# Kernel optimization log

Hardware: AMD Instinct MI355X
Metric: run time of the kernel (lower is better)

## Reference

```python
import jax, jax.numpy as jnp
import numpy as np

F = 8        # number of fields
N_SEQ = 2    # first N_SEQ fields are sequence features
B = 4096     # batch
L = 50       # sequence length for sequence fields
V = 100000   # vocab per field
E = 64       # emb_dim


def setup_inputs() -> dict:
    key = jax.random.key(0)
    k1, k2, k3 = jax.random.split(key, 3)
    x_seq = jax.random.randint(k1, (N_SEQ, B, L), 0, V)          # sequence field inputs
    x_cat = jax.random.randint(k2, (F - N_SEQ, B, 1), 0, V)      # categorical field inputs
    # packed pair-wise tables: tables[a, t] is the embedding table for field a
    # when interacting with target field t (diagonal a==t is unused).
    # RandomNormal(stddev=0.01) initializer in the original.
    tables = jax.random.normal(k3, (F, F, V, E), dtype=jnp.float32) * 0.01
    return {"x_seq": x_seq, "x_cat": x_cat, "tables": tables}


def _pooled(tables, x_seq, x_cat):
    # P[a, t] in [B, E]: field a's input embedded with table (a -> t),
    # mean-pooled over the sequence axis (keepdims semantics folded in).
    P = []
    for a in range(F):  # small fixed loop over fields (structurally distinct inputs)
        idx = x_seq[a] if a < N_SEQ else x_cat[a - N_SEQ]   # [B, La]
        emb = jnp.take(tables[a], idx, axis=1)              # [F, B, La, E]
        P.append(emb.mean(axis=2))                          # [F, B, E]
    return jnp.stack(P)                                     # [F(src), F(tgt), B, E]


def reference(x_seq, x_cat, tables):
    P = _pooled(tables, x_seq, x_cat)
    iu, ju = np.triu_indices(F, k=1)  # all unordered field pairs (a < b)
    # sum over pairs of <emb_{a->b}(x_a), emb_{b->a}(x_b)>
    out = jnp.einsum('pbe,pbe->b', P[iu, ju], P[ju, iu])     # [B]
    return out[:, None, None]                                # [B, 1, 1], matching tf.matmul output
```

## Files before the change

### kernel.cpp

```cpp
#include <hip/hip_runtime.h>

#define FQ 8
#define NSEQ 2
#define BQ 4096
#define LQ 50
#define VQ 100000
#define EQ 64
#define NPAIR 28
#define CQ 4
#define CHUNKS (BQ / CQ)

__device__ const int PA[NPAIR] = {0,0,0,0,0,0,0, 1,1,1,1,1,1, 2,2,2,2,2, 3,3,3,3, 4,4,4, 5,5, 6};
__device__ const int PB[NPAIR] = {1,2,3,4,5,6,7, 2,3,4,5,6,7, 3,4,5,6,7, 4,5,6,7, 5,6,7, 6,7, 7};

template <bool ATOMIC>
__global__ __launch_bounds__(256) void pair_pool_dot(
    const int* __restrict__ x_seq,
    const int* __restrict__ x_cat,
    const float* __restrict__ tables,
    float* __restrict__ partial,
    float* __restrict__ out)
{
    const int blk   = blockIdx.x;
    const int pair  = blk / CHUNKS;
    const int chunk = blk - pair * CHUNKS;
    const int b0    = chunk * CQ;
    const int a = PA[pair], c = PB[pair];
    const int tid  = threadIdx.x;
    const int lane = tid & 63;
    const int wave = tid >> 6;
    const int b    = b0 + wave;

    __shared__ int sidx[2][CQ][LQ];

    if (a < NSEQ) {
        if (tid < CQ * LQ) {
            int bl = tid / LQ, l = tid - bl * LQ;
            sidx[0][bl][l] = x_seq[((size_t)a * BQ + b0 + bl) * LQ + l];
        }
    }
    if (c < NSEQ) {
        if (tid < CQ * LQ) {
            int bl = tid / LQ, l = tid - bl * LQ;
            sidx[1][bl][l] = x_seq[((size_t)c * BQ + b0 + bl) * LQ + l];
        }
    }
    if (a < NSEQ || c < NSEQ) __syncthreads();

    const float* __restrict__ tab1 = tables + ((size_t)a * FQ + c) * VQ * EQ;
    const float* __restrict__ tab2 = tables + ((size_t)c * FQ + a) * VQ * EQ;

    float va, vc;
    if (a < NSEQ) {
        float acc = 0.0f;
        #pragma unroll 10
        for (int l = 0; l < LQ; ++l)
            acc += tab1[(size_t)sidx[0][wave][l] * EQ + lane];
        va = acc * (1.0f / LQ);
    } else {
        int v = x_cat[(size_t)(a - NSEQ) * BQ + b];
        va = tab1[(size_t)v * EQ + lane];
    }
    if (c < NSEQ) {
        float acc = 0.0f;
        #pragma unroll 10
        for (int l = 0; l < LQ; ++l)
            acc += tab2[(size_t)sidx[1][wave][l] * EQ + lane];
        vc = acc * (1.0f / LQ);
    } else {
        int v = x_cat[(size_t)(c - NSEQ) * BQ + b];
        vc = tab2[(size_t)v * EQ + lane];
    }

    float prod = va * vc;
    #pragma unroll
    for (int off = 32; off; off >>= 1)
        prod += __shfl_down(prod, off, 64);
    if (lane == 0) {
        if (ATOMIC) atomicAdd(&out[b], prod);
        else        partial[(size_t)pair * BQ + b] = prod;
    }
}

__global__ __launch_bounds__(256) void reduce_pairs(
    const float* __restrict__ partial, float* __restrict__ out)
{
    int b = blockIdx.x * 256 + threadIdx.x;
    if (b < BQ) {
        float s = 0.0f;
        #pragma unroll
        for (int p = 0; p < NPAIR; ++p)
            s += partial[(size_t)p * BQ + b];
        out[b] = s;
    }
}

__global__ __launch_bounds__(256) void zero_out(float* __restrict__ out)
{
    int b = blockIdx.x * 256 + threadIdx.x;
    if (b < BQ) out[b] = 0.0f;
}

extern "C" void kernel_launch(void* const* d_in, const int* in_sizes, int n_in,
                              void* d_out, int out_size, void* d_ws, size_t ws_size,
                              hipStream_t stream) {
    const int*   x_seq  = (const int*)d_in[0];
    const int*   x_cat  = (const int*)d_in[1];
    const float* tables = (const float*)d_in[2];
    float*       out    = (float*)d_out;

    const size_t need = (size_t)NPAIR * BQ * sizeof(float);
    if (ws_size >= need) {
        float* partial = (float*)d_ws;
        pair_pool_dot<false><<<NPAIR * CHUNKS, 256, 0, stream>>>(
            x_seq, x_cat, tables, partial, out);
        reduce_pairs<<<(BQ + 255) / 256, 256, 0, stream>>>(partial, out);
    } else {
        zero_out<<<(BQ + 255) / 256, 256, 0, stream>>>(out);
        pair_pool_dot<true><<<NPAIR * CHUNKS, 256, 0, stream>>>(
            x_seq, x_cat, tables, nullptr, out);
    }
}
```

Baseline: 119.4 us.

## Vectorize embedding gathers with float4 and split sequence positions across lane groups

New measurement: 117.5 us. About the same (-1.6%).

```diff
diff --git a/kernel.cpp b/kernel.cpp
--- a/kernel.cpp
+++ b/kernel.cpp
@@ -10,11 +10,25 @@
 #define CQ 4
 #define CHUNKS (BQ / CQ)
 
+typedef float f32x4 __attribute__((ext_vector_type(4)));
+
 __device__ const int PA[NPAIR] = {0,0,0,0,0,0,0, 1,1,1,1,1,1, 2,2,2,2,2, 3,3,3,3, 4,4,4, 5,5, 6};
 __device__ const int PB[NPAIR] = {1,2,3,4,5,6,7, 2,3,4,5,6,7, 3,4,5,6,7, 4,5,6,7, 5,6,7, 6,7, 7};
 
+__device__ __forceinline__ f32x4 shflxor4(f32x4 v, int m) {
+    f32x4 r;
+    r.x = __shfl_xor(v.x, m, 64);
+    r.y = __shfl_xor(v.y, m, 64);
+    r.z = __shfl_xor(v.z, m, 64);
+    r.w = __shfl_xor(v.w, m, 64);
+    return r;
+}
+__device__ __forceinline__ float dot4(f32x4 a, f32x4 b) {
+    return a.x*b.x + a.y*b.y + a.z*b.z + a.w*b.w;
+}
+
 template <bool ATOMIC>
-__global__ __launch_bounds__(256) void pair_pool_dot(
+__global__ __launch_bounds__(256) void pair_pool_dot4(
     const int* __restrict__ x_seq,
     const int* __restrict__ x_cat,
     const float* __restrict__ tables,
@@ -29,56 +43,70 @@
     const int tid  = threadIdx.x;
     const int lane = tid & 63;
     const int wave = tid >> 6;
+    const int sub  = lane & 15;
+    const int grp  = lane >> 4;
     const int b    = b0 + wave;
 
     __shared__ int sidx[2][CQ][LQ];
 
-    if (a < NSEQ) {
-        if (tid < CQ * LQ) {
-            int bl = tid / LQ, l = tid - bl * LQ;
-            sidx[0][bl][l] = x_seq[((size_t)a * BQ + b0 + bl) * LQ + l];
-        }
+    if (a < NSEQ && tid < CQ * LQ) {
+        int bl = tid / LQ, l = tid - bl * LQ;
+        sidx[0][bl][l] = x_seq[((size_t)a * BQ + b0 + bl) * LQ + l];
     }
-    if (c < NSEQ) {
-        if (tid < CQ * LQ) {
-            int bl = tid / LQ, l = tid - bl * LQ;
-            sidx[1][bl][l] = x_seq[((size_t)c * BQ + b0 + bl) * LQ + l];
-        }
+    if (c < NSEQ && tid < CQ * LQ) {
+        int bl = tid / LQ, l = tid - bl * LQ;
+        sidx[1][bl][l] = x_seq[((size_t)c * BQ + b0 + bl) * LQ + l];
     }
     if (a < NSEQ || c < NSEQ) __syncthreads();
 
     const float* __restrict__ tab1 = tables + ((size_t)a * FQ + c) * VQ * EQ;
     const float* __restrict__ tab2 = tables + ((size_t)c * FQ + a) * VQ * EQ;
 
-    float va, vc;
-    if (a < NSEQ) {
-        float acc = 0.0f;
-        #pragma unroll 10
-        for (int l = 0; l < LQ; ++l)
-            acc += tab1[(size_t)sidx[0][wave][l] * EQ + lane];
-        va = acc * (1.0f / LQ);
+    float result;
+    if (c < NSEQ) {
+        f32x4 A = {0.f, 0.f, 0.f, 0.f}, B = {0.f, 0.f, 0.f, 0.f};
+        for (int l = grp; l < LQ; l += 4)
+            A += *(const f32x4*)(tab1 + (size_t)sidx[0][wave][l] * EQ + sub * 4);
+        for (int l = grp; l < LQ; l += 4)
+            B += *(const f32x4*)(tab2 + (size_t)sidx[1][wave][l] * EQ + sub * 4);
+        A += shflxor4(A, 16);  A += shflxor4(A, 32);
+        B += shflxor4(B, 16);  B += shflxor4(B, 32);
+        float p = dot4(A, B);
+        p += __shfl_xor(p, 1, 64);
+        p += __shfl_xor(p, 2, 64);
+        p += __shfl_xor(p, 4, 64);
+        p += __shfl_xor(p, 8, 64);
+        result = p * (1.0f / (LQ * LQ));
+    } else if (a < NSEQ) {
+        f32x4 A = {0.f, 0.f, 0.f, 0.f};
+        for (int l = grp; l < LQ; l += 4)
+            A += *(const f32x4*)(tab1 + (size_t)sidx[0][wave][l] * EQ + sub * 4);
+        int vq = x_cat[(size_t)(c - NSEQ) * BQ + b];
+        f32x4 C = *(const f32x4*)(tab2 + (size_t)vq * EQ + sub * 4);
+        float p = dot4(A, C);
+        p += __shfl_xor(p, 1, 64);
+        p += __shfl_xor(p, 2, 64);
+        p += __shfl_xor(p, 4, 64);
+        p += __shfl_xor(p, 8, 64);
+        p += __shfl_xor(p, 16, 64);
+        p += __shfl_xor(p, 32, 64);
+        result = p * (1.0f / LQ);
     } else {
-        int v = x_cat[(size_t)(a - NSEQ) * BQ + b];
-        va = tab1[(size_t)v * EQ + lane];
-    }
-    if (c < NSEQ) {
-        float acc = 0.0f;
-        #pragma unroll 10
-        for (int l = 0; l < LQ; ++l)
-            acc += tab2[(size_t)sidx[1][wave][l] * EQ + lane];
-        vc = acc * (1.0f / LQ);
-    } else {
-        int v = x_cat[(size_t)(c - NSEQ) * BQ + b];
-        vc = tab2[(size_t)v * EQ + lane];
+        int va_i = x_cat[(size_t)(a - NSEQ) * BQ + b];
+        int vc_i = x_cat[(size_t)(c - NSEQ) * BQ + b];
+        f32x4 A = *(const f32x4*)(tab1 + (size_t)va_i * EQ + sub * 4);
+        f32x4 C = *(const f32x4*)(tab2 + (size_t)vc_i * EQ + sub * 4);
+        float p = dot4(A, C);
+        p += __shfl_xor(p, 1, 64);
+        p += __shfl_xor(p, 2, 64);
+        p += __shfl_xor(p, 4, 64);
+        p += __shfl_xor(p, 8, 64);
+        result = p;
     }
 
-    float prod = va * vc;
-    #pragma unroll
-    for (int off = 32; off; off >>= 1)
-        prod += __shfl_down(prod, off, 64);
     if (lane == 0) {
-        if (ATOMIC) atomicAdd(&out[b], prod);
-        else        partial[(size_t)pair * BQ + b] = prod;
+        if (ATOMIC) atomicAdd(&out[b], result);
+        else        partial[(size_t)pair * BQ + b] = result;
     }
 }
 
@@ -112,12 +140,12 @@
     const size_t need = (size_t)NPAIR * BQ * sizeof(float);
     if (ws_size >= need) {
         float* partial = (float*)d_ws;
-        pair_pool_dot<false><<<NPAIR * CHUNKS, 256, 0, stream>>>(
+        pair_pool_dot4<false><<<NPAIR * CHUNKS, 256, 0, stream>>>(
             x_seq, x_cat, tables, partial, out);
         reduce_pairs<<<(BQ + 255) / 256, 256, 0, stream>>>(partial, out);
     } else {
         zero_out<<<(BQ + 255) / 256, 256, 0, stream>>>(out);
-        pair_pool_dot<true><<<NPAIR * CHUNKS, 256, 0, stream>>>(
+        pair_pool_dot4<true><<<NPAIR * CHUNKS, 256, 0, stream>>>(
             x_seq, x_cat, tables, nullptr, out);
     }
 }
```
